# Optimization experiments

Measured on AMD Instinct MI355X. Metric: run time of the kernel, lower is better.

The kernel has to match this reference:

```python
import jax, jax.numpy as jnp
import numpy as np

B, T, D = 4, 2048, 1024

def setup_inputs() -> dict:
    key = jax.random.key(0)
    kx, kq, kk, kv = jax.random.split(key, 4)
    return {
        "vector": jax.random.normal(kx, (B, T, D), dtype=jnp.float32),
        # original uses torch.rand -> uniform [0,1)
        "W_queries": jax.random.uniform(kq, (D, D), dtype=jnp.float32),
        "W_keys": jax.random.uniform(kk, (D, D), dtype=jnp.float32),
        "W_values": jax.random.uniform(kv, (D, D), dtype=jnp.float32),
    }

def reference(vector, W_queries, W_keys, W_values):
    b, num_token, d_out = vector.shape
    queries = vector @ W_queries          # [b, t, d]
    keys = vector @ W_keys                # [b, t, d]
    values = vector @ W_values            # [b, t, d]
    # attention_score: [b, q, k]
    scores = jnp.einsum('bqd,bkd->bqk', queries, keys)
    causal_mask = jnp.triu(jnp.ones((num_token, num_token), dtype=bool), k=1)
    scores = jnp.where(causal_mask[None, :, :], -jnp.inf, scores)
    # NOTE: original uses FLOOR division `//` by sqrt(d_k) -- faithful here.
    inv_sqrt_scale = jnp.asarray(np.sqrt(keys.shape[-1]), dtype=scores.dtype)
    weights = jnp.floor(scores / inv_sqrt_scale)
    # NOTE: original applies softmax over dim=1 (the query axis), not dim=-1.
    weights = jax.nn.softmax(weights, axis=1)
    # dropout rate is 0.0 (eval/deterministic): identity
    context = jnp.einsum('bqk,bkd->bqd', weights, values)
    return context
```

## Files before the change

### kernel.cpp

```cpp
#include <hip/hip_runtime.h>
#include <math.h>

typedef _Float16 half4 __attribute__((ext_vector_type(4)));
typedef _Float16 half8 __attribute__((ext_vector_type(8)));
typedef float f32x4 __attribute__((ext_vector_type(4)));

#define GLD16(gptr, lptr)                                                     \
    __builtin_amdgcn_global_load_lds(                                         \
        (const __attribute__((address_space(1))) unsigned int*)(gptr),        \
        (__attribute__((address_space(3))) unsigned int*)(lptr), 16, 0, 0)

namespace {

constexpr int Bb = 4;
constexpr int Tt = 2048;
constexpr int Dd = 1024;
constexpr int BT = Bb * Tt;
constexpr int NCH = 16;

__device__ inline _Float16 f2h(float f) { return (_Float16)f; }

__global__ __launch_bounds__(256) void convert_x_kernel(
    const float* __restrict__ X, _Float16* __restrict__ Xhi, _Float16* __restrict__ Xlo)
{
    const int idx = (blockIdx.x * 256 + threadIdx.x) * 4;
    const float4 v = *(const float4*)(X + idx);
    const float a[4] = {v.x, v.y, v.z, v.w};
    half4 h, l;
#pragma unroll
    for (int i = 0; i < 4; ++i) {
        h[i] = f2h(a[i]);
        l[i] = f2h(a[i] - (float)h[i]);
    }
    *(half4*)(Xhi + idx) = h;
    *(half4*)(Xlo + idx) = l;
}

__global__ __launch_bounds__(256) void convert_wqk_kernel(
    const float* __restrict__ Wq, const float* __restrict__ Wk,
    _Float16* __restrict__ Wqh, _Float16* __restrict__ Wql,
    _Float16* __restrict__ Wkh, _Float16* __restrict__ Wkl)
{
    const int mat = blockIdx.y;
    const float* W = mat ? Wk : Wq;
    _Float16* Hh = mat ? Wkh : Wqh;
    _Float16* Ll = mat ? Wkl : Wql;
    const int idx = (blockIdx.x * 256 + threadIdx.x) * 4;
    const float4 v = *(const float4*)(W + idx);
    const float a[4] = {v.x, v.y, v.z, v.w};
    half4 h, l;
#pragma unroll
    for (int i = 0; i < 4; ++i) {
        h[i] = f2h(a[i]);
        l[i] = f2h(a[i] - (float)h[i]);
    }
    *(half4*)(Hh + idx) = h;
    *(half4*)(Ll + idx) = l;
}

__global__ __launch_bounds__(256) void convert_wv_kernel(
    const float* __restrict__ Wv, _Float16* __restrict__ WvTh)
{
    __shared__ float tile[64][65];
    const int n0 = blockIdx.x * 64, k0 = blockIdx.y * 64;
    const int tx = threadIdx.x & 63, ty = threadIdx.x >> 6;
#pragma unroll
    for (int i = 0; i < 16; ++i)
        tile[ty + i * 4][tx] = Wv[(size_t)(k0 + ty + i * 4) * Dd + n0 + tx];
    __syncthreads();
#pragma unroll
    for (int i = 0; i < 16; ++i) {
        const float v = tile[tx][ty + i * 4];
        WvTh[(size_t)(n0 + ty + i * 4) * Dd + k0 + tx] = f2h(v);
    }
}

__global__ __launch_bounds__(256) void gt_kernel(
    const _Float16* __restrict__ Wkh, const _Float16* __restrict__ Wkl,
    const _Float16* __restrict__ Wqh, const _Float16* __restrict__ Wql,
    _Float16* __restrict__ GTh, _Float16* __restrict__ GTl)
{
    __shared__ _Float16 Ahl[2][4][512];
    __shared__ _Float16 Bhl[2][4][512];

    const int n0 = blockIdx.x * 64;
    const int m0 = blockIdx.y * 64;
    const int tid = threadIdx.x;
    const int w = tid >> 6, lane = tid & 63;
    const int lr = lane & 15, lq = lane >> 4;
    const int wi = (w >> 1) * 2, wj = (w & 1) * 2;

    f32x4 acc[2][2];
#pragma unroll
    for (int i = 0; i < 2; ++i)
#pragma unroll
        for (int j = 0; j < 2; ++j)
#pragma unroll
            for (int c = 0; c < 4; ++c) acc[i][j][c] = 0.f;

    for (int kk = 0; kk < 1024; kk += 32) {
        __syncthreads();
        {
            const int s = w;
            const size_t ar = (size_t)(m0 + s * 16 + lr) * Dd + kk + lq * 8;
            const size_t br = (size_t)(n0 + s * 16 + lr) * Dd + kk + lq * 8;
            GLD16(Wkh + ar, &Ahl[0][s][0]);
            GLD16(Wkl + ar, &Ahl[1][s][0]);
            GLD16(Wqh + br, &Bhl[0][s][0]);
            GLD16(Wql + br, &Bhl[1][s][0]);
        }
        __syncthreads();
        half8 ah[2], al[2], bh[2], bl[2];
#pragma unroll
        for (int i = 0; i < 2; ++i) {
            ah[i] = *(const half8*)&Ahl[0][wi + i][lane * 8];
            al[i] = *(const half8*)&Ahl[1][wi + i][lane * 8];
        }
#pragma unroll
        for (int j = 0; j < 2; ++j) {
            bh[j] = *(const half8*)&Bhl[0][wj + j][lane * 8];
            bl[j] = *(const half8*)&Bhl[1][wj + j][lane * 8];
        }
#pragma unroll
        for (int i = 0; i < 2; ++i)
#pragma unroll
            for (int j = 0; j < 2; ++j) {
                acc[i][j] = __builtin_amdgcn_mfma_f32_16x16x32_f16(ah[i], bh[j], acc[i][j], 0, 0, 0);
                acc[i][j] = __builtin_amdgcn_mfma_f32_16x16x32_f16(ah[i], bl[j], acc[i][j], 0, 0, 0);
                acc[i][j] = __builtin_amdgcn_mfma_f32_16x16x32_f16(al[i], bh[j], acc[i][j], 0, 0, 0);
            }
    }

#pragma unroll
    for (int i = 0; i < 2; ++i)
#pragma unroll
        for (int r = 0; r < 4; ++r) {
            const int row = m0 + (wi + i) * 16 + lq * 4 + r;
#pragma unroll
            for (int j = 0; j < 2; ++j) {
                const int col = n0 + (wj + j) * 16 + lr;
                const float v = acc[i][j][r];
                const _Float16 h = f2h(v);
                GTh[(size_t)row * Dd + col] = h;
                GTl[(size_t)row * Dd + col] = f2h(v - (float)h);
            }
        }
}

__global__ __launch_bounds__(256) void t_kernel(
    const _Float16* __restrict__ Xhi, const _Float16* __restrict__ Xlo,
    const _Float16* __restrict__ GTh, const _Float16* __restrict__ GTl,
    _Float16* __restrict__ Thi, _Float16* __restrict__ Tlo)
{
    __shared__ _Float16 Ahl[2][8][512];
    __shared__ _Float16 Bhl[2][8][512];

    const int n0 = blockIdx.x * 128;
    const int m0 = blockIdx.y * 128;
    const int tid = threadIdx.x;
    const int w = tid >> 6, lane = tid & 63;
    const int lr = lane & 15, lq = lane >> 4;
    const int wr = (w >> 1) * 4, wc = (w & 1) * 4;

    f32x4 acc[4][4];
#pragma unroll
    for (int i = 0; i < 4; ++i)
#pragma unroll
        for (int j = 0; j < 4; ++j)
#pragma unroll
            for (int c = 0; c < 4; ++c) acc[i][j][c] = 0.f;

    for (int kk = 0; kk < 1024; kk += 32) {
        __syncthreads();
#pragma unroll
        for (int s2 = 0; s2 < 2; ++s2) {
            const int s = w * 2 + s2;
            const size_t ar = (size_t)(m0 + s * 16 + lr) * Dd + kk + lq * 8;
            const size_t br = (size_t)(n0 + s * 16 + lr) * Dd + kk + lq * 8;
            GLD16(Xhi + ar, &Ahl[0][s][0]);
            GLD16(Xlo + ar, &Ahl[1][s][0]);
            GLD16(GTh + br, &Bhl[0][s][0]);
            GLD16(GTl + br, &Bhl[1][s][0]);
        }
        __syncthreads();
        half8 ah[4], al[4], bh[4], bl[4];
#pragma unroll
        for (int i = 0; i < 4; ++i) {
            ah[i] = *(const half8*)&Ahl[0][wr + i][lane * 8];
            al[i] = *(const half8*)&Ahl[1][wr + i][lane * 8];
        }
#pragma unroll
        for (int j = 0; j < 4; ++j) {
            bh[j] = *(const half8*)&Bhl[0][wc + j][lane * 8];
            bl[j] = *(const half8*)&Bhl[1][wc + j][lane * 8];
        }
#pragma unroll
        for (int i = 0; i < 4; ++i)
#pragma unroll
            for (int j = 0; j < 4; ++j) {
                acc[i][j] = __builtin_amdgcn_mfma_f32_16x16x32_f16(ah[i], bh[j], acc[i][j], 0, 0, 0);
                acc[i][j] = __builtin_amdgcn_mfma_f32_16x16x32_f16(ah[i], bl[j], acc[i][j], 0, 0, 0);
                acc[i][j] = __builtin_amdgcn_mfma_f32_16x16x32_f16(al[i], bh[j], acc[i][j], 0, 0, 0);
            }
    }
#pragma unroll
    for (int i = 0; i < 4; ++i)
#pragma unroll
        for (int r = 0; r < 4; ++r) {
            const int row = m0 + (wr + i) * 16 + lq * 4 + r;
#pragma unroll
            for (int j = 0; j < 4; ++j) {
                const int col = n0 + (wc + j) * 16 + lr;
                const float v = acc[i][j][r];
                const _Float16 h = f2h(v);
                Thi[(size_t)row * Dd + col] = h;
                Tlo[(size_t)row * Dd + col] = f2h(v - (float)h);
            }
        }
}

__global__ __launch_bounds__(256) void v_kernel(
    const _Float16* __restrict__ Xhi, const _Float16* __restrict__ WvTh,
    _Float16* __restrict__ Vrow)
{
    __shared__ _Float16 Al[8][512];
    __shared__ _Float16 Bl[8][512];

    const int n0 = blockIdx.x * 128;
    const int m0 = blockIdx.y * 128;
    const int tid = threadIdx.x;
    const int w = tid >> 6, lane = tid & 63;
    const int lr = lane & 15, lq = lane >> 4;
    const int wr = (w >> 1) * 4, wc = (w & 1) * 4;

    f32x4 acc[4][4];
#pragma unroll
    for (int i = 0; i < 4; ++i)
#pragma unroll
        for (int j = 0; j < 4; ++j)
#pragma unroll
            for (int c = 0; c < 4; ++c) acc[i][j][c] = 0.f;

    for (int kk = 0; kk < 1024; kk += 32) {
        __syncthreads();
#pragma unroll
        for (int s2 = 0; s2 < 2; ++s2) {
            const int s = w * 2 + s2;
            GLD16(Xhi + (size_t)(m0 + s * 16 + lr) * Dd + kk + lq * 8, &Al[s][0]);
            GLD16(WvTh + (size_t)(n0 + s * 16 + lr) * Dd + kk + lq * 8, &Bl[s][0]);
        }
        __syncthreads();
        half8 a[4], b2[4];
#pragma unroll
        for (int i = 0; i < 4; ++i) a[i] = *(const half8*)&Al[wr + i][lane * 8];
#pragma unroll
        for (int j = 0; j < 4; ++j) b2[j] = *(const half8*)&Bl[wc + j][lane * 8];
#pragma unroll
        for (int i = 0; i < 4; ++i)
#pragma unroll
            for (int j = 0; j < 4; ++j)
                acc[i][j] = __builtin_amdgcn_mfma_f32_16x16x32_f16(a[i], b2[j], acc[i][j], 0, 0, 0);
    }
#pragma unroll
    for (int i = 0; i < 4; ++i)
#pragma unroll
        for (int r = 0; r < 4; ++r) {
            const int row = m0 + (wr + i) * 16 + lq * 4 + r;
#pragma unroll
            for (int j = 0; j < 4; ++j)
                Vrow[(size_t)row * Dd + n0 + (wc + j) * 16 + lr] = f2h(acc[i][j][r]);
        }
}

__global__ __launch_bounds__(256) void transpose_v_kernel(
    const _Float16* __restrict__ Vrow, const float* __restrict__ Lb,
    _Float16* __restrict__ Vt)
{
    __shared__ _Float16 tile[64][78];
    const int d0 = blockIdx.x * 64, t0 = blockIdx.y * 64, b = blockIdx.z;
    const int tx = threadIdx.x & 63, ty = threadIdx.x >> 6;
#pragma unroll
    for (int i = 0; i < 16; ++i)
        tile[ty + i * 4][tx] = Vrow[((size_t)b * Tt + t0 + ty + i * 4) * Dd + d0 + tx];
    __syncthreads();
    const float sc = Lb[(size_t)b * Tt + t0 + tx];
#pragma unroll
    for (int i = 0; i < 16; ++i) {
        const float v = (float)tile[tx][ty + i * 4] * sc;
        Vt[(size_t)b * Dd * Tt + (size_t)(d0 + ty + i * 4) * Tt + t0 + tx] = f2h(v);
    }
}

__global__ __launch_bounds__(256) void scores_mfma_kernel(
    const _Float16* __restrict__ Thi, const _Float16* __restrict__ Tlo,
    const _Float16* __restrict__ Xhi, const _Float16* __restrict__ Xlo,
    float* __restrict__ S, float* __restrict__ Pm, float* __restrict__ Pl)
{
    const int t = blockIdx.x;
    int byi = (int)((sqrtf(8.f * t + 1.f) - 1.f) * 0.5f);
    if ((byi + 1) * (byi + 2) / 2 <= t) ++byi;
    if (byi * (byi + 1) / 2 > t) --byi;
    const int bxi = t - byi * (byi + 1) / 2;
    const int b = blockIdx.z;
    const int j0 = bxi * 128, q0 = byi * 128;
    float* Sb = S + (size_t)b * Tt * Tt;

    __shared__ _Float16 Ahl[2][8][512];
    __shared__ _Float16 Bhl[2][8][512];
    const _Float16* Th = Thi + (size_t)b * Tt * Dd;
    const _Float16* Tl = Tlo + (size_t)b * Tt * Dd;
    const _Float16* Xh = Xhi + (size_t)b * Tt * Dd;
    const _Float16* Xl = Xlo + (size_t)b * Tt * Dd;

    const int tid = threadIdx.x;
    const int w = tid >> 6, lane = tid & 63;
    const int lr = lane & 15, lq = lane >> 4;
    const int wr = (w >> 1) * 4, wc = (w & 1) * 4;

    f32x4 acc[4][4];
#pragma unroll
    for (int i = 0; i < 4; ++i)
#pragma unroll
        for (int j = 0; j < 4; ++j)
#pragma unroll
            for (int c = 0; c < 4; ++c) acc[i][j][c] = 0.f;

    for (int kk = 0; kk < 1024; kk += 32) {
        __syncthreads();
#pragma unroll
        for (int s2 = 0; s2 < 2; ++s2) {
            const int s = w * 2 + s2;
            const size_t ar = (size_t)(q0 + s * 16 + lr) * Dd + kk + lq * 8;
            const size_t br = (size_t)(j0 + s * 16 + lr) * Dd + kk + lq * 8;
            GLD16(Th + ar, &Ahl[0][s][0]);
            GLD16(Tl + ar, &Ahl[1][s][0]);
            GLD16(Xh + br, &Bhl[0][s][0]);
            GLD16(Xl + br, &Bhl[1][s][0]);
        }
        __syncthreads();
        half8 ah[4], al[4], bh[4], bl[4];
#pragma unroll
        for (int i = 0; i < 4; ++i) {
            ah[i] = *(const half8*)&Ahl[0][wr + i][lane * 8];
            al[i] = *(const half8*)&Ahl[1][wr + i][lane * 8];
        }
#pragma unroll
        for (int j = 0; j < 4; ++j) {
            bh[j] = *(const half8*)&Bhl[0][wc + j][lane * 8];
            bl[j] = *(const half8*)&Bhl[1][wc + j][lane * 8];
        }
#pragma unroll
        for (int i = 0; i < 4; ++i)
#pragma unroll
            for (int j = 0; j < 4; ++j) {
                acc[i][j] = __builtin_amdgcn_mfma_f32_16x16x32_f16(ah[i], bh[j], acc[i][j], 0, 0, 0);
                acc[i][j] = __builtin_amdgcn_mfma_f32_16x16x32_f16(ah[i], bl[j], acc[i][j], 0, 0, 0);
                acc[i][j] = __builtin_amdgcn_mfma_f32_16x16x32_f16(al[i], bh[j], acc[i][j], 0, 0, 0);
            }
    }

    float sv[4][4][4];
#pragma unroll
    for (int i = 0; i < 4; ++i)
#pragma unroll
        for (int r = 0; r < 4; ++r) {
            const int q = q0 + (wr + i) * 16 + lq * 4 + r;
#pragma unroll
            for (int j = 0; j < 4; ++j) {
                const int jg = j0 + (wc + j) * 16 + lr;
                const float v = (jg <= q) ? floorf(acc[i][j][r] * 0.03125f) : -INFINITY;
                sv[i][j][r] = v;
                Sb[(size_t)q * Tt + jg] = v;
            }
        }

    float* red  = (float*)&Ahl[0][0][0];
    float* colm = red + 2048;
    __syncthreads();
    for (int e = tid; e < 2048; e += 256) red[e] = -INFINITY;
    __syncthreads();
    const int rowidx = (w * 4 + lq) * 128;
#pragma unroll
    for (int j = 0; j < 4; ++j) {
        const int c = (wc + j) * 16 + lr;
        float lm = -INFINITY;
#pragma unroll
        for (int i = 0; i < 4; ++i)
#pragma unroll
            for (int r = 0; r < 4; ++r) lm = fmaxf(lm, sv[i][j][r]);
        red[rowidx + c] = lm;
    }
    __syncthreads();
    if (tid < 128) {
        float m = -INFINITY;
#pragma unroll
        for (int e = 0; e < 16; ++e) m = fmaxf(m, red[e * 128 + tid]);
        colm[tid] = m;
    }
    __syncthreads();
    float ls[4];
#pragma unroll
    for (int j = 0; j < 4; ++j) {
        const int c = (wc + j) * 16 + lr;
        const float m = colm[c];
        float s = 0.f;
#pragma unroll
        for (int i = 0; i < 4; ++i)
#pragma unroll
            for (int r = 0; r < 4; ++r)
                if (sv[i][j][r] != -INFINITY) s += __expf(sv[i][j][r] - m);
        ls[j] = s;
    }
    __syncthreads();
    for (int e = tid; e < 2048; e += 256) red[e] = 0.f;
    __syncthreads();
#pragma unroll
    for (int j = 0; j < 4; ++j) red[rowidx + (wc + j) * 16 + lr] = ls[j];
    __syncthreads();
    if (tid < 128) {
        float l = 0.f;
#pragma unroll
        for (int e = 0; e < 16; ++e) l += red[e * 128 + tid];
        const size_t o = ((size_t)b * NCH + byi) * Tt + j0 + tid;
        Pm[o] = colm[tid];
        Pl[o] = l;
    }
}

__global__ __launch_bounds__(256) void colstats_merge_kernel(
    const float* __restrict__ Pm, const float* __restrict__ Pl,
    float* __restrict__ Mb, float* __restrict__ Lb)
{
    const int j = blockIdx.x * 256 + threadIdx.x;
    const int b = blockIdx.y;
    const int jt = j >> 7;
    float m = -INFINITY, l = 0.f;
    for (int c = jt; c < NCH; ++c) {
        const size_t pidx = ((size_t)b * NCH + c) * Tt + j;
        const float mi = Pm[pidx];
        if (mi == -INFINITY) continue;
        const float li = Pl[pidx];
        if (mi > m) { l = l * __expf(m - mi) + li; m = mi; }
        else        { l += li * __expf(mi - m); }
    }
    Mb[(size_t)b * Tt + j] = m;
    Lb[(size_t)b * Tt + j] = (l > 0.f) ? 1.f / l : 0.f;
}

__global__ __launch_bounds__(256) void pmat_kernel(
    const float* __restrict__ S, const float* __restrict__ Mb,
    _Float16* __restrict__ P)
{
    const int t = blockIdx.x;
    int byi = (int)((sqrtf(8.f * t + 1.f) - 1.f) * 0.5f);
    if ((byi + 1) * (byi + 2) / 2 <= t) ++byi;
    if (byi * (byi + 1) / 2 > t) --byi;
    const int bxi = t - byi * (byi + 1) / 2;
    const int b = blockIdx.z;
    const int j0 = bxi * 128, q0 = byi * 128;

    const int tr = threadIdx.x >> 4;
    const int tc = (threadIdx.x & 15) * 8;
    const float* mp = Mb + (size_t)b * Tt + j0 + tc;
    float mv[8];
#pragma unroll
    for (int e = 0; e < 8; ++e) mv[e] = mp[e];

#pragma unroll
    for (int it = 0; it < 8; ++it) {
        const int row = q0 + it * 16 + tr;
        const float* Sp = S + (size_t)b * Tt * Tt + (size_t)row * Tt + j0 + tc;
        const float4 s0 = *(const float4*)Sp;
        const float4 s1 = *(const float4*)(Sp + 4);
        const float sa[8] = {s0.x, s0.y, s0.z, s0.w, s1.x, s1.y, s1.z, s1.w};
        half8 out;
#pragma unroll
        for (int e = 0; e < 8; ++e) {
            const int jg = j0 + tc + e;
            out[e] = (jg <= row) ? f2h(__expf(sa[e] - mv[e])) : (_Float16)0.f;
        }
        *(half8*)(P + (size_t)b * Tt * Tt + (size_t)row * Tt + j0 + tc) = out;
    }
}

__global__ __launch_bounds__(256) void context_mfma_kernel(
    const _Float16* __restrict__ P, const _Float16* __restrict__ Vt,
    float* __restrict__ Out)
{
    __shared__ _Float16 Al[8][512];
    __shared__ _Float16 Bl[8][512];

    const int bx = blockIdx.x;
    const int by = (int)gridDim.y - 1 - blockIdx.y;
    const int b  = blockIdx.z;
    const int d0 = bx * 128;
    const int q0 = by * 128;
    const _Float16* Pb = P + (size_t)b * Tt * Tt;
    const _Float16* Vb = Vt + (size_t)b * Dd * Tt;
    float* Ob = Out + (size_t)b * Tt * Dd;

    const int tid = threadIdx.x;
    const int w = tid >> 6, lane = tid & 63;
    const int lr = lane & 15, lq = lane >> 4;
    const int wr = (w >> 1) * 4, wc = (w & 1) * 4;

    f32x4 acc[4][4];
#pragma unroll
    for (int i = 0; i < 4; ++i)
#pragma unroll
        for (int j = 0; j < 4; ++j)
#pragma unroll
            for (int c = 0; c < 4; ++c) acc[i][j][c] = 0.f;

    const int kmax = q0 + 128;
    for (int k0 = 0; k0 < kmax; k0 += 32) {
        __syncthreads();
#pragma unroll
        for (int s2 = 0; s2 < 2; ++s2) {
            const int s = w * 2 + s2;
            GLD16(Pb + (size_t)(q0 + s * 16 + lr) * Tt + k0 + lq * 8, &Al[s][0]);
            GLD16(Vb + (size_t)(d0 + s * 16 + lr) * Tt + k0 + lq * 8, &Bl[s][0]);
        }
        __syncthreads();
        half8 a[4], b2[4];
#pragma unroll
        for (int i = 0; i < 4; ++i) a[i] = *(const half8*)&Al[wr + i][lane * 8];
#pragma unroll
        for (int j = 0; j < 4; ++j) b2[j] = *(const half8*)&Bl[wc + j][lane * 8];
#pragma unroll
        for (int i = 0; i < 4; ++i)
#pragma unroll
            for (int j = 0; j < 4; ++j)
                acc[i][j] = __builtin_amdgcn_mfma_f32_16x16x32_f16(a[i], b2[j], acc[i][j], 0, 0, 0);
    }

#pragma unroll
    for (int i = 0; i < 4; ++i)
#pragma unroll
        for (int r = 0; r < 4; ++r) {
            const int row = q0 + (wr + i) * 16 + lq * 4 + r;
#pragma unroll
            for (int j = 0; j < 4; ++j)
                Ob[(size_t)row * Dd + d0 + (wc + j) * 16 + lr] = acc[i][j][r];
        }
}

}

extern "C" void kernel_launch(void* const* d_in, const int* in_sizes, int n_in,
                              void* d_out, int out_size, void* d_ws, size_t ws_size,
                              hipStream_t stream)
{
    const float* X  = (const float*)d_in[0];
    const float* Wq = (const float*)d_in[1];
    const float* Wk = (const float*)d_in[2];
    const float* Wv = (const float*)d_in[3];

    char* ws = (char*)d_ws;
    const size_t MB = 1024 * 1024;
    _Float16* Xhi  = (_Float16*)ws;
    _Float16* Xlo  = (_Float16*)(ws + 16 * MB);
    _Float16* Wqh  = (_Float16*)(ws + 32 * MB);
    _Float16* Wql  = (_Float16*)(ws + 34 * MB);
    _Float16* Wkh  = (_Float16*)(ws + 36 * MB);
    _Float16* Wkl  = (_Float16*)(ws + 38 * MB);
    _Float16* WvTh = (_Float16*)(ws + 40 * MB);
    _Float16* GTh  = (_Float16*)(ws + 44 * MB);
    _Float16* GTl  = (_Float16*)(ws + 46 * MB);
    _Float16* Thi  = (_Float16*)(ws + 48 * MB);
    _Float16* Tlo  = (_Float16*)(ws + 64 * MB);
    _Float16* P    = Thi;
    _Float16* Vt   = (_Float16*)(ws + 80 * MB);
    _Float16* Vrow = (_Float16*)(ws + 96 * MB);
    float*    S    = (float*)(ws + 112 * MB);
    float*    Mb   = (float*)(ws + 176 * MB);
    float*    Lb   = Mb + (size_t)Bb * Tt;
    float*    Pm   = Lb + (size_t)Bb * Tt;
    float*    Pl   = Pm + (size_t)Bb * NCH * Tt;
    float*    Out  = (float*)d_out;

    convert_x_kernel<<<BT * Dd / 1024, 256, 0, stream>>>(X, Xhi, Xlo);
    convert_wqk_kernel<<<dim3(Dd * Dd / 1024, 2), 256, 0, stream>>>(Wq, Wk, Wqh, Wql, Wkh, Wkl);
    convert_wv_kernel<<<dim3(16, 16), 256, 0, stream>>>(Wv, WvTh);
    gt_kernel<<<dim3(16, 16), 256, 0, stream>>>(Wkh, Wkl, Wqh, Wql, GTh, GTl);
    t_kernel<<<dim3(8, 64), 256, 0, stream>>>(Xhi, Xlo, GTh, GTl, Thi, Tlo);
    v_kernel<<<dim3(8, 64), 256, 0, stream>>>(Xhi, WvTh, Vrow);
    scores_mfma_kernel<<<dim3(136, 1, Bb), 256, 0, stream>>>(Thi, Tlo, Xhi, Xlo, S, Pm, Pl);
    colstats_merge_kernel<<<dim3(Tt / 256, Bb), 256, 0, stream>>>(Pm, Pl, Mb, Lb);
    transpose_v_kernel<<<dim3(Dd / 64, Tt / 64, Bb), 256, 0, stream>>>(Vrow, Lb, Vt);
    pmat_kernel<<<dim3(136, 1, Bb), 256, 0, stream>>>(S, Mb, P);
    context_mfma_kernel<<<dim3(Dd / 128, Tt / 128, Bb), 256, 0, stream>>>(P, Vt, Out);
}
```

Measured before the change: 457.0 us.

## Fuse exp into scores kernel with per-chunk local max and correction factors

The scores kernel now writes exp(s - local column max) as fp16 P directly, dropping the fp32 S matrix and the separate pmat kernel. The merge kernel emits a per-(row-chunk, column) correction factor exp(m_local - m_global), and the context kernel multiplies each loaded P fragment by it. This removes a full fp32 T×T write and read plus one launch, at the cost of extra per-iteration multiplies in the context kernel and fp16 range risk for local-max-relative values.

```diff
diff --git a/kernel.cpp b/kernel.cpp
--- a/kernel.cpp
+++ b/kernel.cpp
@@ -294,7 +294,7 @@
 __global__ __launch_bounds__(256) void scores_mfma_kernel(
     const _Float16* __restrict__ Thi, const _Float16* __restrict__ Tlo,
     const _Float16* __restrict__ Xhi, const _Float16* __restrict__ Xlo,
-    float* __restrict__ S, float* __restrict__ Pm, float* __restrict__ Pl)
+    _Float16* __restrict__ P, float* __restrict__ Pm, float* __restrict__ Pl)
 {
     const int t = blockIdx.x;
     int byi = (int)((sqrtf(8.f * t + 1.f) - 1.f) * 0.5f);
@@ -303,7 +303,7 @@
     const int bxi = t - byi * (byi + 1) / 2;
     const int b = blockIdx.z;
     const int j0 = bxi * 128, q0 = byi * 128;
-    float* Sb = S + (size_t)b * Tt * Tt;
+    _Float16* Pb = P + (size_t)b * Tt * Tt;
 
     __shared__ _Float16 Ahl[2][8][512];
     __shared__ _Float16 Bhl[2][8][512];
@@ -368,9 +368,7 @@
 #pragma unroll
             for (int j = 0; j < 4; ++j) {
                 const int jg = j0 + (wc + j) * 16 + lr;
-                const float v = (jg <= q) ? floorf(acc[i][j][r] * 0.03125f) : -INFINITY;
-                sv[i][j][r] = v;
-                Sb[(size_t)q * Tt + jg] = v;
+                sv[i][j][r] = (jg <= q) ? floorf(acc[i][j][r] * 0.03125f) : -INFINITY;
             }
         }
 
@@ -398,17 +396,23 @@
         colm[tid] = m;
     }
     __syncthreads();
+
     float ls[4];
 #pragma unroll
     for (int j = 0; j < 4; ++j) {
         const int c = (wc + j) * 16 + lr;
         const float m = colm[c];
+        const int jg = j0 + c;
         float s = 0.f;
 #pragma unroll
         for (int i = 0; i < 4; ++i)
 #pragma unroll
-            for (int r = 0; r < 4; ++r)
-                if (sv[i][j][r] != -INFINITY) s += __expf(sv[i][j][r] - m);
+            for (int r = 0; r < 4; ++r) {
+                const float e = __expf(sv[i][j][r] - m);
+                s += e;
+                const int q = q0 + (wr + i) * 16 + lq * 4 + r;
+                Pb[(size_t)q * Tt + jg] = f2h(e);
+            }
         ls[j] = s;
     }
     __syncthreads();
@@ -429,7 +433,7 @@
 
 __global__ __launch_bounds__(256) void colstats_merge_kernel(
     const float* __restrict__ Pm, const float* __restrict__ Pl,
-    float* __restrict__ Mb, float* __restrict__ Lb)
+    float* __restrict__ Lb, _Float16* __restrict__ Cc)
 {
     const int j = blockIdx.x * 256 + threadIdx.x;
     const int b = blockIdx.y;
@@ -443,49 +447,16 @@
         if (mi > m) { l = l * __expf(m - mi) + li; m = mi; }
         else        { l += li * __expf(mi - m); }
     }
-    Mb[(size_t)b * Tt + j] = m;
     Lb[(size_t)b * Tt + j] = (l > 0.f) ? 1.f / l : 0.f;
-}
-
-__global__ __launch_bounds__(256) void pmat_kernel(
-    const float* __restrict__ S, const float* __restrict__ Mb,
-    _Float16* __restrict__ P)
-{
-    const int t = blockIdx.x;
-    int byi = (int)((sqrtf(8.f * t + 1.f) - 1.f) * 0.5f);
-    if ((byi + 1) * (byi + 2) / 2 <= t) ++byi;
-    if (byi * (byi + 1) / 2 > t) --byi;
-    const int bxi = t - byi * (byi + 1) / 2;
-    const int b = blockIdx.z;
-    const int j0 = bxi * 128, q0 = byi * 128;
-
-    const int tr = threadIdx.x >> 4;
-    const int tc = (threadIdx.x & 15) * 8;
-    const float* mp = Mb + (size_t)b * Tt + j0 + tc;
-    float mv[8];
-#pragma unroll
-    for (int e = 0; e < 8; ++e) mv[e] = mp[e];
-
-#pragma unroll
-    for (int it = 0; it < 8; ++it) {
-        const int row = q0 + it * 16 + tr;
-        const float* Sp = S + (size_t)b * Tt * Tt + (size_t)row * Tt + j0 + tc;
-        const float4 s0 = *(const float4*)Sp;
-        const float4 s1 = *(const float4*)(Sp + 4);
-        const float sa[8] = {s0.x, s0.y, s0.z, s0.w, s1.x, s1.y, s1.z, s1.w};
-        half8 out;
-#pragma unroll
-        for (int e = 0; e < 8; ++e) {
-            const int jg = j0 + tc + e;
-            out[e] = (jg <= row) ? f2h(__expf(sa[e] - mv[e])) : (_Float16)0.f;
-        }
-        *(half8*)(P + (size_t)b * Tt * Tt + (size_t)row * Tt + j0 + tc) = out;
+    for (int c = jt; c < NCH; ++c) {
+        const size_t pidx = ((size_t)b * NCH + c) * Tt + j;
+        Cc[pidx] = f2h(__expf(Pm[pidx] - m));
     }
 }
 
 __global__ __launch_bounds__(256) void context_mfma_kernel(
     const _Float16* __restrict__ P, const _Float16* __restrict__ Vt,
-    float* __restrict__ Out)
+    const _Float16* __restrict__ Cc, float* __restrict__ Out)
 {
     __shared__ _Float16 Al[8][512];
     __shared__ _Float16 Bl[8][512];
@@ -497,6 +468,7 @@
     const int q0 = by * 128;
     const _Float16* Pb = P + (size_t)b * Tt * Tt;
     const _Float16* Vb = Vt + (size_t)b * Dd * Tt;
+    const _Float16* Ccb = Cc + ((size_t)b * NCH + by) * Tt;
     float* Ob = Out + (size_t)b * Tt * Dd;
 
     const int tid = threadIdx.x;
@@ -522,9 +494,10 @@
             GLD16(Vb + (size_t)(d0 + s * 16 + lr) * Tt + k0 + lq * 8, &Bl[s][0]);
         }
         __syncthreads();
+        const half8 cf = *(const half8*)(Ccb + k0 + lq * 8);
         half8 a[4], b2[4];
 #pragma unroll
-        for (int i = 0; i < 4; ++i) a[i] = *(const half8*)&Al[wr + i][lane * 8];
+        for (int i = 0; i < 4; ++i) a[i] = *(const half8*)&Al[wr + i][lane * 8] * cf;
 #pragma unroll
         for (int j = 0; j < 4; ++j) b2[j] = *(const half8*)&Bl[wc + j][lane * 8];
 #pragma unroll
@@ -569,14 +542,13 @@
     _Float16* GTl  = (_Float16*)(ws + 46 * MB);
     _Float16* Thi  = (_Float16*)(ws + 48 * MB);
     _Float16* Tlo  = (_Float16*)(ws + 64 * MB);
-    _Float16* P    = Thi;
     _Float16* Vt   = (_Float16*)(ws + 80 * MB);
     _Float16* Vrow = (_Float16*)(ws + 96 * MB);
-    float*    S    = (float*)(ws + 112 * MB);
-    float*    Mb   = (float*)(ws + 176 * MB);
-    float*    Lb   = Mb + (size_t)Bb * Tt;
+    _Float16* P    = (_Float16*)(ws + 112 * MB);
+    float*    Lb   = (float*)(ws + 176 * MB);
     float*    Pm   = Lb + (size_t)Bb * Tt;
     float*    Pl   = Pm + (size_t)Bb * NCH * Tt;
+    _Float16* Cc   = (_Float16*)(Pl + (size_t)Bb * NCH * Tt);
     float*    Out  = (float*)d_out;
 
     convert_x_kernel<<<BT * Dd / 1024, 256, 0, stream>>>(X, Xhi, Xlo);
@@ -585,9 +557,8 @@
     gt_kernel<<<dim3(16, 16), 256, 0, stream>>>(Wkh, Wkl, Wqh, Wql, GTh, GTl);
     t_kernel<<<dim3(8, 64), 256, 0, stream>>>(Xhi, Xlo, GTh, GTl, Thi, Tlo);
     v_kernel<<<dim3(8, 64), 256, 0, stream>>>(Xhi, WvTh, Vrow);
-    scores_mfma_kernel<<<dim3(136, 1, Bb), 256, 0, stream>>>(Thi, Tlo, Xhi, Xlo, S, Pm, Pl);
-    colstats_merge_kernel<<<dim3(Tt / 256, Bb), 256, 0, stream>>>(Pm, Pl, Mb, Lb);
+    scores_mfma_kernel<<<dim3(136, 1, Bb), 256, 0, stream>>>(Thi, Tlo, Xhi, Xlo, P, Pm, Pl);
+    colstats_merge_kernel<<<dim3(Tt / 256, Bb), 256, 0, stream>>>(Pm, Pl, Lb, Cc);
     transpose_v_kernel<<<dim3(Dd / 64, Tt / 64, Bb), 256, 0, stream>>>(Vrow, Lb, Vt);
-    pmat_kernel<<<dim3(136, 1, Bb), 256, 0, stream>>>(S, Mb, P);
-    context_mfma_kernel<<<dim3(Dd / 128, Tt / 128, Bb), 256, 0, stream>>>(P, Vt, Out);
-}
+    context_mfma_kernel<<<dim3(Dd / 128, Tt / 128, Bb), 256, 0, stream>>>(P, Vt, Cc, Out);
+}
```

Measured after the change: 470.8 us. +3.0%, slower.

## Fuse T/V GEMMs and weight converts, remap blocks for XCD-local L2 reuse

Applied to the files above, without the earlier changes.

Merges the Wq/Wk split-conversion and the Wv transpose-conversion into one launch. Merges the T and V projection GEMMs into a single 1024-block launch whose block index is swizzled so blocks sharing X rows land on the same XCD. Replaces the triangular block decode in the scores kernel with an XCD-aware pairing of short and long rows, balancing work per XCD and improving L2 locality. The goals are fewer launches, a better tail and better cache reuse. The cost is divergent block roles and more complex indexing.

```diff
diff --git a/kernel.cpp b/kernel.cpp
--- a/kernel.cpp
+++ b/kernel.cpp
@@ -36,42 +36,43 @@
     *(half4*)(Xlo + idx) = l;
 }
 
-__global__ __launch_bounds__(256) void convert_wqk_kernel(
+__global__ __launch_bounds__(256) void convert_w_kernel(
     const float* __restrict__ Wq, const float* __restrict__ Wk,
+    const float* __restrict__ Wv,
     _Float16* __restrict__ Wqh, _Float16* __restrict__ Wql,
-    _Float16* __restrict__ Wkh, _Float16* __restrict__ Wkl)
-{
-    const int mat = blockIdx.y;
-    const float* W = mat ? Wk : Wq;
-    _Float16* Hh = mat ? Wkh : Wqh;
-    _Float16* Ll = mat ? Wkl : Wql;
-    const int idx = (blockIdx.x * 256 + threadIdx.x) * 4;
-    const float4 v = *(const float4*)(W + idx);
-    const float a[4] = {v.x, v.y, v.z, v.w};
-    half4 h, l;
-#pragma unroll
-    for (int i = 0; i < 4; ++i) {
-        h[i] = f2h(a[i]);
-        l[i] = f2h(a[i] - (float)h[i]);
-    }
-    *(half4*)(Hh + idx) = h;
-    *(half4*)(Ll + idx) = l;
-}
-
-__global__ __launch_bounds__(256) void convert_wv_kernel(
-    const float* __restrict__ Wv, _Float16* __restrict__ WvTh)
-{
-    __shared__ float tile[64][65];
-    const int n0 = blockIdx.x * 64, k0 = blockIdx.y * 64;
-    const int tx = threadIdx.x & 63, ty = threadIdx.x >> 6;
-#pragma unroll
-    for (int i = 0; i < 16; ++i)
-        tile[ty + i * 4][tx] = Wv[(size_t)(k0 + ty + i * 4) * Dd + n0 + tx];
-    __syncthreads();
-#pragma unroll
-    for (int i = 0; i < 16; ++i) {
-        const float v = tile[tx][ty + i * 4];
-        WvTh[(size_t)(n0 + ty + i * 4) * Dd + k0 + tx] = f2h(v);
+    _Float16* __restrict__ Wkh, _Float16* __restrict__ Wkl,
+    _Float16* __restrict__ WvTh)
+{
+    const int y = blockIdx.y;
+    if (y < 2) {
+        const float* W = y ? Wk : Wq;
+        _Float16* Hh = y ? Wkh : Wqh;
+        _Float16* Ll = y ? Wkl : Wql;
+        const int idx = (blockIdx.x * 256 + threadIdx.x) * 4;
+        const float4 v = *(const float4*)(W + idx);
+        const float a[4] = {v.x, v.y, v.z, v.w};
+        half4 h, l;
+#pragma unroll
+        for (int i = 0; i < 4; ++i) {
+            h[i] = f2h(a[i]);
+            l[i] = f2h(a[i] - (float)h[i]);
+        }
+        *(half4*)(Hh + idx) = h;
+        *(half4*)(Ll + idx) = l;
+    } else {
+        if (blockIdx.x >= 256) return;
+        __shared__ float tile[64][65];
+        const int n0 = (blockIdx.x & 15) * 64, k0 = (blockIdx.x >> 4) * 64;
+        const int tx = threadIdx.x & 63, ty = threadIdx.x >> 6;
+#pragma unroll
+        for (int i = 0; i < 16; ++i)
+            tile[ty + i * 4][tx] = Wv[(size_t)(k0 + ty + i * 4) * Dd + n0 + tx];
+        __syncthreads();
+#pragma unroll
+        for (int i = 0; i < 16; ++i) {
+            const float v = tile[tx][ty + i * 4];
+            WvTh[(size_t)(n0 + ty + i * 4) * Dd + k0 + tx] = f2h(v);
+        }
     }
 }
 
@@ -147,16 +148,23 @@
         }
 }
 
-__global__ __launch_bounds__(256) void t_kernel(
+__global__ __launch_bounds__(256) void tv_kernel(
     const _Float16* __restrict__ Xhi, const _Float16* __restrict__ Xlo,
     const _Float16* __restrict__ GTh, const _Float16* __restrict__ GTl,
-    _Float16* __restrict__ Thi, _Float16* __restrict__ Tlo)
-{
-    __shared__ _Float16 Ahl[2][8][512];
-    __shared__ _Float16 Bhl[2][8][512];
-
-    const int n0 = blockIdx.x * 128;
-    const int m0 = blockIdx.y * 128;
+    const _Float16* __restrict__ WvTh,
+    _Float16* __restrict__ Thi, _Float16* __restrict__ Tlo,
+    _Float16* __restrict__ Vrow)
+{
+    __shared__ _Float16 smem[16384];
+
+    const int lb = blockIdx.x;
+    const int xcd = lb & 7, sl = lb >> 3;
+    const int g = xcd + 8 * (sl >> 4);
+    const int tn = sl & 15;
+    const bool isT = tn < 8;
+    const int n0 = (tn & 7) * 128;
+    const int m0 = g * 128;
+
     const int tid = threadIdx.x;
     const int w = tid >> 6, lane = tid & 63;
     const int lr = lane & 15, lq = lane >> 4;
@@ -170,106 +178,85 @@
 #pragma unroll
             for (int c = 0; c < 4; ++c) acc[i][j][c] = 0.f;
 
-    for (int kk = 0; kk < 1024; kk += 32) {
-        __syncthreads();
-#pragma unroll
-        for (int s2 = 0; s2 < 2; ++s2) {
-            const int s = w * 2 + s2;
-            const size_t ar = (size_t)(m0 + s * 16 + lr) * Dd + kk + lq * 8;
-            const size_t br = (size_t)(n0 + s * 16 + lr) * Dd + kk + lq * 8;
-            GLD16(Xhi + ar, &Ahl[0][s][0]);
-            GLD16(Xlo + ar, &Ahl[1][s][0]);
-            GLD16(GTh + br, &Bhl[0][s][0]);
-            GLD16(GTl + br, &Bhl[1][s][0]);
-        }
-        __syncthreads();
-        half8 ah[4], al[4], bh[4], bl[4];
-#pragma unroll
-        for (int i = 0; i < 4; ++i) {
-            ah[i] = *(const half8*)&Ahl[0][wr + i][lane * 8];
-            al[i] = *(const half8*)&Ahl[1][wr + i][lane * 8];
-        }
-#pragma unroll
-        for (int j = 0; j < 4; ++j) {
-            bh[j] = *(const half8*)&Bhl[0][wc + j][lane * 8];
-            bl[j] = *(const half8*)&Bhl[1][wc + j][lane * 8];
+    if (isT) {
+        for (int kk = 0; kk < 1024; kk += 32) {
+            __syncthreads();
+#pragma unroll
+            for (int s2 = 0; s2 < 2; ++s2) {
+                const int s = w * 2 + s2;
+                const size_t ar = (size_t)(m0 + s * 16 + lr) * Dd + kk + lq * 8;
+                const size_t br = (size_t)(n0 + s * 16 + lr) * Dd + kk + lq * 8;
+                GLD16(Xhi + ar, smem + s * 512);
+                GLD16(Xlo + ar, smem + 4096 + s * 512);
+                GLD16(GTh + br, smem + 8192 + s * 512);
+                GLD16(GTl + br, smem + 12288 + s * 512);
+            }
+            __syncthreads();
+            half8 ah[4], al[4], bh[4], bl[4];
+#pragma unroll
+            for (int i = 0; i < 4; ++i) {
+                ah[i] = *(const half8*)&smem[(wr + i) * 512 + lane * 8];
+                al[i] = *(const half8*)&smem[4096 + (wr + i) * 512 + lane * 8];
+            }
+#pragma unroll
+            for (int j = 0; j < 4; ++j) {
+                bh[j] = *(const half8*)&smem[8192 + (wc + j) * 512 + lane * 8];
+                bl[j] = *(const half8*)&smem[12288 + (wc + j) * 512 + lane * 8];
+            }
+#pragma unroll
+            for (int i = 0; i < 4; ++i)
+#pragma unroll
+                for (int j = 0; j < 4; ++j) {
+                    acc[i][j] = __builtin_amdgcn_mfma_f32_16x16x32_f16(ah[i], bh[j], acc[i][j], 0, 0, 0);
+                    acc[i][j] = __builtin_amdgcn_mfma_f32_16x16x32_f16(ah[i], bl[j], acc[i][j], 0, 0, 0);
+                    acc[i][j] = __builtin_amdgcn_mfma_f32_16x16x32_f16(al[i], bh[j], acc[i][j], 0, 0, 0);
+                }
         }
 #pragma unroll
         for (int i = 0; i < 4; ++i)
 #pragma unroll
-            for (int j = 0; j < 4; ++j) {
-                acc[i][j] = __builtin_amdgcn_mfma_f32_16x16x32_f16(ah[i], bh[j], acc[i][j], 0, 0, 0);
-                acc[i][j] = __builtin_amdgcn_mfma_f32_16x16x32_f16(ah[i], bl[j], acc[i][j], 0, 0, 0);
-                acc[i][j] = __builtin_amdgcn_mfma_f32_16x16x32_f16(al[i], bh[j], acc[i][j], 0, 0, 0);
-            }
-    }
-#pragma unroll
-    for (int i = 0; i < 4; ++i)
-#pragma unroll
-        for (int r = 0; r < 4; ++r) {
-            const int row = m0 + (wr + i) * 16 + lq * 4 + r;
-#pragma unroll
-            for (int j = 0; j < 4; ++j) {
-                const int col = n0 + (wc + j) * 16 + lr;
-                const float v = acc[i][j][r];
-                const _Float16 h = f2h(v);
-                Thi[(size_t)row * Dd + col] = h;
-                Tlo[(size_t)row * Dd + col] = f2h(v - (float)h);
-            }
-        }
-}
-
-__global__ __launch_bounds__(256) void v_kernel(
-    const _Float16* __restrict__ Xhi, const _Float16* __restrict__ WvTh,
-    _Float16* __restrict__ Vrow)
-{
-    __shared__ _Float16 Al[8][512];
-    __shared__ _Float16 Bl[8][512];
-
-    const int n0 = blockIdx.x * 128;
-    const int m0 = blockIdx.y * 128;
-    const int tid = threadIdx.x;
-    const int w = tid >> 6, lane = tid & 63;
-    const int lr = lane & 15, lq = lane >> 4;
-    const int wr = (w >> 1) * 4, wc = (w & 1) * 4;
-
-    f32x4 acc[4][4];
-#pragma unroll
-    for (int i = 0; i < 4; ++i)
-#pragma unroll
-        for (int j = 0; j < 4; ++j)
-#pragma unroll
-            for (int c = 0; c < 4; ++c) acc[i][j][c] = 0.f;
-
-    for (int kk = 0; kk < 1024; kk += 32) {
-        __syncthreads();
-#pragma unroll
-        for (int s2 = 0; s2 < 2; ++s2) {
-            const int s = w * 2 + s2;
-            GLD16(Xhi + (size_t)(m0 + s * 16 + lr) * Dd + kk + lq * 8, &Al[s][0]);
-            GLD16(WvTh + (size_t)(n0 + s * 16 + lr) * Dd + kk + lq * 8, &Bl[s][0]);
-        }
-        __syncthreads();
-        half8 a[4], b2[4];
-#pragma unroll
-        for (int i = 0; i < 4; ++i) a[i] = *(const half8*)&Al[wr + i][lane * 8];
-#pragma unroll
-        for (int j = 0; j < 4; ++j) b2[j] = *(const half8*)&Bl[wc + j][lane * 8];
+            for (int r = 0; r < 4; ++r) {
+                const int row = m0 + (wr + i) * 16 + lq * 4 + r;
+#pragma unroll
+                for (int j = 0; j < 4; ++j) {
+                    const int col = n0 + (wc + j) * 16 + lr;
+                    const float v = acc[i][j][r];
+                    const _Float16 h = f2h(v);
+                    Thi[(size_t)row * Dd + col] = h;
+                    Tlo[(size_t)row * Dd + col] = f2h(v - (float)h);
+                }
+            }
+    } else {
+        for (int kk = 0; kk < 1024; kk += 32) {
+            __syncthreads();
+#pragma unroll
+            for (int s2 = 0; s2 < 2; ++s2) {
+                const int s = w * 2 + s2;
+                GLD16(Xhi + (size_t)(m0 + s * 16 + lr) * Dd + kk + lq * 8, smem + s * 512);
+                GLD16(WvTh + (size_t)(n0 + s * 16 + lr) * Dd + kk + lq * 8, smem + 8192 + s * 512);
+            }
+            __syncthreads();
+            half8 a[4], b2[4];
+#pragma unroll
+            for (int i = 0; i < 4; ++i) a[i] = *(const half8*)&smem[(wr + i) * 512 + lane * 8];
+#pragma unroll
+            for (int j = 0; j < 4; ++j) b2[j] = *(const half8*)&smem[8192 + (wc + j) * 512 + lane * 8];
+#pragma unroll
+            for (int i = 0; i < 4; ++i)
+#pragma unroll
+                for (int j = 0; j < 4; ++j)
+                    acc[i][j] = __builtin_amdgcn_mfma_f32_16x16x32_f16(a[i], b2[j], acc[i][j], 0, 0, 0);
+        }
 #pragma unroll
         for (int i = 0; i < 4; ++i)
 #pragma unroll
-            for (int j = 0; j < 4; ++j)
-                acc[i][j] = __builtin_amdgcn_mfma_f32_16x16x32_f16(a[i], b2[j], acc[i][j], 0, 0, 0);
-    }
-#pragma unroll
-    for (int i = 0; i < 4; ++i)
-#pragma unroll
-        for (int r = 0; r < 4; ++r) {
-            const int row = m0 + (wr + i) * 16 + lq * 4 + r;
-#pragma unroll
-            for (int j = 0; j < 4; ++j)
-                Vrow[(size_t)row * Dd + n0 + (wc + j) * 16 + lr] = f2h(acc[i][j][r]);
-        }
+            for (int r = 0; r < 4; ++r) {
+                const int row = m0 + (wr + i) * 16 + lq * 4 + r;
+#pragma unroll
+                for (int j = 0; j < 4; ++j)
+                    Vrow[(size_t)row * Dd + n0 + (wc + j) * 16 + lr] = f2h(acc[i][j][r]);
+            }
+    }
 }
 
 __global__ __launch_bounds__(256) void transpose_v_kernel(
@@ -296,11 +283,11 @@
     const _Float16* __restrict__ Xhi, const _Float16* __restrict__ Xlo,
     float* __restrict__ S, float* __restrict__ Pm, float* __restrict__ Pl)
 {
-    const int t = blockIdx.x;
-    int byi = (int)((sqrtf(8.f * t + 1.f) - 1.f) * 0.5f);
-    if ((byi + 1) * (byi + 2) / 2 <= t) ++byi;
-    if (byi * (byi + 1) / 2 > t) --byi;
-    const int bxi = t - byi * (byi + 1) / 2;
+    const int r0i = blockIdx.x;
+    const int xcd = r0i & 7, sl = r0i >> 3;
+    int byi, bxi;
+    if (sl <= xcd) { byi = xcd;      bxi = sl; }
+    else           { byi = 15 - xcd; bxi = sl - xcd - 1; }
     const int b = blockIdx.z;
     const int j0 = bxi * 128, q0 = byi * 128;
     float* Sb = S + (size_t)b * Tt * Tt;
@@ -580,11 +567,10 @@
     float*    Out  = (float*)d_out;
 
     convert_x_kernel<<<BT * Dd / 1024, 256, 0, stream>>>(X, Xhi, Xlo);
-    convert_wqk_kernel<<<dim3(Dd * Dd / 1024, 2), 256, 0, stream>>>(Wq, Wk, Wqh, Wql, Wkh, Wkl);
-    convert_wv_kernel<<<dim3(16, 16), 256, 0, stream>>>(Wv, WvTh);
+    convert_w_kernel<<<dim3(Dd * Dd / 1024, 3), 256, 0, stream>>>(
+        Wq, Wk, Wv, Wqh, Wql, Wkh, Wkl, WvTh);
     gt_kernel<<<dim3(16, 16), 256, 0, stream>>>(Wkh, Wkl, Wqh, Wql, GTh, GTl);
-    t_kernel<<<dim3(8, 64), 256, 0, stream>>>(Xhi, Xlo, GTh, GTl, Thi, Tlo);
-    v_kernel<<<dim3(8, 64), 256, 0, stream>>>(Xhi, WvTh, Vrow);
+    tv_kernel<<<dim3(1024), 256, 0, stream>>>(Xhi, Xlo, GTh, GTl, WvTh, Thi, Tlo, Vrow);
     scores_mfma_kernel<<<dim3(136, 1, Bb), 256, 0, stream>>>(Thi, Tlo, Xhi, Xlo, S, Pm, Pl);
     colstats_merge_kernel<<<dim3(Tt / 256, Bb), 256, 0, stream>>>(Pm, Pl, Mb, Lb);
     transpose_v_kernel<<<dim3(Dd / 64, Tt / 64, Bb), 256, 0, stream>>>(Vrow, Lb, Vt);
```

Result: no change. 463.6 us (+1.5%).
